# Optimization experiments

Hardware: AMD Instinct MI355X
Metric: run time of the kernel (lower is better)

The kernel has to match this reference:

```python
import jax, jax.numpy as jnp
import numpy as np

N = 50000          # num nodes
NUM_HE = 10000     # num hyperedges
E = 800000         # num graph edges
INC = 800000       # num (node, hyperedge) incidences
IN_C, HID, OUT_C = 128, 128, 64
SLOPE = 0.01       # torch leaky_relu default negative slope


def _leaky(x):
    return jnp.where(x >= 0, x, SLOPE * x)


def hypergraph_conv(x, he_index, theta, bias):
    # PyG HypergraphConv (no attention, unit hyperedge weights):
    # out = D^{-1} H B^{-1} H^T (X Theta) + bias
    node_idx, he_idx = he_index[0], he_index[1]
    x = x @ theta                                            # [N, F]
    ones = jnp.ones(node_idx.shape[0], x.dtype)
    D = jax.ops.segment_sum(ones, node_idx, num_segments=N)           # node degree
    B = jax.ops.segment_sum(ones, he_idx, num_segments=NUM_HE)        # hyperedge degree
    Dinv = jnp.where(D > 0, 1.0 / D, 0.0)
    Binv = jnp.where(B > 0, 1.0 / B, 0.0)
    # node -> hyperedge
    m = jax.ops.segment_sum(x[node_idx], he_idx, num_segments=NUM_HE) * Binv[:, None]
    # hyperedge -> node
    out = jax.ops.segment_sum(m[he_idx], node_idx, num_segments=N) * Dinv[:, None]
    return out + bias


def graph_conv(x, edge_index, w_rel, b_rel, w_root):
    # PyG GraphConv (aggr='add'): out_i = W_rel * sum_{j->i} x_j + b_rel + W_root * x_i
    src, dst = edge_index[0], edge_index[1]
    agg = jax.ops.segment_sum(x[src], dst, num_segments=N)
    return agg @ w_rel + b_rel + x @ w_root


def _forward(X, edge_index, hyperedge_index,
             hc1_w, hc1_b, lin1_w, lin1_b,
             hc2_w, hc2_b, lin2_w, lin2_b,
             c1_wrel, c1_brel, c1_wroot, glin1_w, glin1_b,
             c2_wrel, c2_brel, c2_wroot, glin2_w, glin2_b,
             fc_w, fc_b):
    # dropout is identity in eval mode (and first two calls in the source discard their output)
    X = _leaky(hypergraph_conv(X, hyperedge_index, hc1_w, hc1_b) + (X @ lin1_w + lin1_b))
    X = _leaky(hypergraph_conv(X, hyperedge_index, hc2_w, hc2_b) + (X @ lin2_w + lin2_b))
    X = _leaky(graph_conv(X, edge_index, c1_wrel, c1_brel, c1_wroot) + (X @ glin1_w + glin1_b))
    X = _leaky(graph_conv(X, edge_index, c2_wrel, c2_brel, c2_wroot) + (X @ glin2_w + glin2_b))
    y = X @ fc_w + fc_b
    return X, y


def setup_inputs() -> dict:
    key = jax.random.key(0)
    ks = jax.random.split(key, 32)
    s = 0.02
    inp = {
        'X': jax.random.normal(ks[0], (N, IN_C), jnp.float32),
        'edge_index': jnp.stack([
            jax.random.randint(ks[1], (E,), 0, N),
            jax.random.randint(ks[2], (E,), 0, N)]).astype(jnp.int64),
        'hyperedge_index': jnp.stack([
            jax.random.randint(ks[3], (INC,), 0, N),
            jax.random.randint(ks[4], (INC,), 0, NUM_HE)]).astype(jnp.int64),
        'hc1_w': jax.random.normal(ks[5], (IN_C, HID), jnp.float32) * s,
        'hc1_b': jnp.zeros((HID,), jnp.float32),
        'lin1_w': jax.random.normal(ks[6], (IN_C, HID), jnp.float32) * s,
        'lin1_b': jnp.zeros((HID,), jnp.float32),
        'hc2_w': jax.random.normal(ks[7], (HID, HID), jnp.float32) * s,
        'hc2_b': jnp.zeros((HID,), jnp.float32),
        'lin2_w': jax.random.normal(ks[8], (HID, HID), jnp.float32) * s,
        'lin2_b': jnp.zeros((HID,), jnp.float32),
        'c1_wrel': jax.random.normal(ks[9], (HID, HID), jnp.float32) * s,
        'c1_brel': jnp.zeros((HID,), jnp.float32),
        'c1_wroot': jax.random.normal(ks[10], (HID, HID), jnp.float32) * s,
        'glin1_w': jax.random.normal(ks[11], (HID, HID), jnp.float32) * s,
        'glin1_b': jnp.zeros((HID,), jnp.float32),
        'c2_wrel': jax.random.normal(ks[12], (HID, HID), jnp.float32) * s,
        'c2_brel': jnp.zeros((HID,), jnp.float32),
        'c2_wroot': jax.random.normal(ks[13], (HID, HID), jnp.float32) * s,
        'glin2_w': jax.random.normal(ks[14], (HID, HID), jnp.float32) * s,
        'glin2_b': jnp.zeros((HID,), jnp.float32),
        'fc_w': jax.random.normal(ks[15], (HID, OUT_C), jnp.float32) * s,
        'fc_b': jnp.zeros((OUT_C,), jnp.float32),
    }
    return inp


def reference(X, edge_index, hyperedge_index,
              hc1_w, hc1_b, lin1_w, lin1_b,
              hc2_w, hc2_b, lin2_w, lin2_b,
              c1_wrel, c1_brel, c1_wroot, glin1_w, glin1_b,
              c2_wrel, c2_brel, c2_wroot, glin2_w, glin2_b,
              fc_w, fc_b):
    return _forward(X, edge_index, hyperedge_index,
                    hc1_w, hc1_b, lin1_w, lin1_b,
                    hc2_w, hc2_b, lin2_w, lin2_b,
                    c1_wrel, c1_brel, c1_wroot, glin1_w, glin1_b,
                    c2_wrel, c2_brel, c2_wroot, glin2_w, glin2_b,
                    fc_w, fc_b)
```

## Files before the change

kernel.cpp:

```cpp
#include <hip/hip_runtime.h>

#define NN 50000
#define HECNT 10000
#define EE 800000
#define II 800000
#define NBK 128
#define CHUNK 4096
#define BKCAP 8192

typedef _Float16 half8 __attribute__((ext_vector_type(8)));
typedef float f32x4    __attribute__((ext_vector_type(4)));

__global__ void detect_k(const int* __restrict__ EIX, const int* __restrict__ HIX,
                         int* __restrict__ flags) {
    __shared__ int o0, o1;
    int tid = threadIdx.x;
    if (tid == 0) { o0 = 0; o1 = 0; }
    __syncthreads();
    atomicOr(&o0, EIX[2 * tid + 1]);
    atomicOr(&o1, HIX[2 * tid + 1]);
    __syncthreads();
    if (tid == 0) { flags[0] = (o0 == 0); flags[1] = (o1 == 0); }
}

__device__ __forceinline__ int ld_idx(const int* p, long long pos, int is64) {
    return is64 ? p[pos * 2] : p[(int)pos];
}

__device__ __forceinline__ void task_info(int t, int& n, int& cbase, int& obase) {
    if (t == 0)      { n = HECNT; cbase = 0;           obase = 0; }
    else if (t == 1) { n = NN;    cbase = HECNT;       obase = HECNT + 1; }
    else             { n = NN;    cbase = HECNT + NN;  obase = HECNT + NN + 2; }
}

__device__ __forceinline__ void ld_edge(int t, long long i,
                                        const int* EIX, const int* HIX,
                                        int f0, int f1, int& d, int& v) {
    int rng;
    if (t == 0)      { d = ld_idx(HIX, (long long)II + i, f1); v = ld_idx(HIX, i, f1); rng = HECNT; }
    else if (t == 1) { d = ld_idx(HIX, i, f1); v = ld_idx(HIX, (long long)II + i, f1); rng = NN; }
    else             { d = ld_idx(EIX, (long long)EE + i, f0); v = ld_idx(EIX, i, f0); rng = NN; }
    if ((unsigned)d >= (unsigned)rng || (unsigned)v >= 65536u) d = -1;
}

__global__ void binit_k(int* __restrict__ bcur) {
    int i = blockIdx.x * 256 + threadIdx.x;
    if (i < 3 * NBK) bcur[i] = i * BKCAP;
}

__global__ __launch_bounds__(256) void bin_k(const int* __restrict__ EIX,
                                             const int* __restrict__ HIX,
                                             const int* __restrict__ flags,
                                             int* __restrict__ bcur,
                                             unsigned* __restrict__ pairs) {
    int t = blockIdx.y;
    __shared__ int hcnt[NBK], hstart[NBK], hrun[NBK], gbase[NBK];
    __shared__ int stot;
    __shared__ unsigned stage[CHUNK];
    int tid = threadIdx.x;
    int n, cb, ob; task_info(t, n, cb, ob);
    int span = (n + NBK - 1) / NBK;
    long long base = (long long)blockIdx.x * CHUNK;
    int f0 = flags[0], f1 = flags[1];

    for (int i = tid; i < NBK; i += 256) { hcnt[i] = 0; hrun[i] = 0; }
    __syncthreads();

    int d[16], v[16], b[16];
    #pragma unroll
    for (int j = 0; j < 16; j++) {
        long long i = base + j * 256 + tid;
        int dd = -1, vv = 0;
        if (i < EE) ld_edge(t, i, EIX, HIX, f0, f1, dd, vv);
        d[j] = dd; v[j] = vv;
        if (dd >= 0) { b[j] = dd / span; atomicAdd(&hcnt[b[j]], 1); }
    }
    __syncthreads();

    if (tid < NBK) gbase[tid] = hcnt[tid] ? atomicAdd(&bcur[t * NBK + tid], hcnt[tid]) : 0;
    if (tid < NBK) hstart[tid] = hcnt[tid];
    __syncthreads();
    for (int o = 1; o < NBK; o <<= 1) {
        int u = 0;
        if (tid < NBK && tid >= o) u = hstart[tid - o];
        __syncthreads();
        if (tid < NBK) hstart[tid] += u;
        __syncthreads();
    }
    if (tid == NBK - 1) stot = hstart[tid];
    __syncthreads();
    if (tid < NBK) hstart[tid] -= hcnt[tid];
    __syncthreads();

    #pragma unroll
    for (int j = 0; j < 16; j++) {
        if (d[j] >= 0) {
            int p = hstart[b[j]] + atomicAdd(&hrun[b[j]], 1);
            stage[p] = ((unsigned)d[j] << 16) | (unsigned)v[j];
        }
    }
    __syncthreads();

    int total = stot;
    for (int i = tid; i < total; i += 256) {
        int lo = 0, hi = NBK - 1;
        while (lo < hi) { int mid = (lo + hi + 1) >> 1; if (hstart[mid] <= i) lo = mid; else hi = mid - 1; }
        int pos = gbase[lo] + (i - hstart[lo]);
        if (pos < (t * NBK + lo + 1) * BKCAP)
            pairs[pos] = stage[i];
    }
}

__global__ __launch_bounds__(256) void count_k(const int* __restrict__ bcur,
                                               const unsigned* __restrict__ pairs,
                                               int* __restrict__ counts) {
    int idx = blockIdx.x;
    int t = idx / NBK, b = idx % NBK;
    int n, cb, ob; task_info(t, n, cb, ob);
    int span = (n + NBK - 1) / NBK;
    int dlo = min(b * span, n), dhi = min(dlo + span, n);
    __shared__ int hist[400];
    int tid = threadIdx.x;
    for (int i = tid; i < dhi - dlo; i += 256) hist[i] = 0;
    __syncthreads();
    int cnt = min(bcur[idx] - idx * BKCAP, BKCAP);
    const unsigned* pw = pairs + (size_t)idx * BKCAP;
    for (int i = tid; i < cnt; i += 256) {
        int dl = (int)(pw[i] >> 16) - dlo;
        if ((unsigned)dl < (unsigned)(dhi - dlo)) atomicAdd(&hist[dl], 1);
    }
    __syncthreads();
    for (int i = tid; i < dhi - dlo; i += 256) counts[cb + dlo + i] = hist[i];
}

__global__ __launch_bounds__(256) void scan_p1(const int* __restrict__ counts,
                                               int* __restrict__ bsums) {
    int t = blockIdx.y;
    int n, cb, ob; task_info(t, n, cb, ob);
    int base = blockIdx.x * 1024 + threadIdx.x * 4;
    int s = 0;
    #pragma unroll
    for (int j = 0; j < 4; j++) { int i = base + j; if (i < n) s += counts[cb + i]; }
    __shared__ int red[256];
    red[threadIdx.x] = s; __syncthreads();
    for (int o = 128; o > 0; o >>= 1) {
        if (threadIdx.x < o) red[threadIdx.x] += red[threadIdx.x + o];
        __syncthreads();
    }
    if (threadIdx.x == 0) bsums[t * 64 + blockIdx.x] = red[0];
}

__global__ void scan_p2(int* __restrict__ bsums, int* __restrict__ offs) {
    int t = blockIdx.y;
    int n, cb, ob; task_info(t, n, cb, ob);
    int lane = threadIdx.x;
    int nb = (n + 1023) / 1024;
    int v = (lane < nb) ? bsums[t * 64 + lane] : 0;
    int incl = v;
    for (int d = 1; d < 64; d <<= 1) {
        int u = __shfl_up(incl, (unsigned)d, 64);
        if (lane >= d) incl += u;
    }
    bsums[t * 64 + lane] = incl - v;
    int total = __shfl(incl, 63, 64);
    if (lane == 0) offs[ob + n] = total;
}

__global__ __launch_bounds__(256) void scan_p3(const int* __restrict__ counts,
                                               const int* __restrict__ bsums,
                                               int* __restrict__ offs) {
    int t = blockIdx.y;
    int n, cb, ob; task_info(t, n, cb, ob);
    int tid = threadIdx.x;
    int base = blockIdx.x * 1024 + tid * 4;
    int c[4]; int s = 0;
    #pragma unroll
    for (int j = 0; j < 4; j++) { int i = base + j; c[j] = (i < n) ? counts[cb + i] : 0; s += c[j]; }
    __shared__ int sc[256];
    sc[tid] = s; __syncthreads();
    for (int o = 1; o < 256; o <<= 1) {
        int v = (tid >= o) ? sc[tid - o] : 0;
        __syncthreads();
        sc[tid] += v;
        __syncthreads();
    }
    int excl = sc[tid] - s;
    int p = bsums[t * 64 + blockIdx.x] + excl;
    #pragma unroll
    for (int j = 0; j < 4; j++) {
        int i = base + j;
        if (i < n) { offs[ob + i] = p; p += c[j]; }
    }
}

__global__ __launch_bounds__(256) void unbin_k(const int* __restrict__ offs,
                                               const unsigned* __restrict__ pairs,
                                               int* __restrict__ vals) {
    int idx = blockIdx.x;
    int t = idx / NBK, b = idx % NBK;
    int n, cb, ob; task_info(t, n, cb, ob);
    int span = (n + NBK - 1) / NBK;
    int dlo = min(b * span, n), dhi = min(dlo + span, n);
    if (dhi <= dlo) return;
    int p0 = offs[ob + dlo], p1 = offs[ob + dhi];
    int cnt = p1 - p0;
    __shared__ int win[BKCAP];
    __shared__ int cur[400];
    int tid = threadIdx.x;
    for (int i = tid; i < dhi - dlo; i += 256) cur[i] = offs[ob + dlo + i] - p0;
    __syncthreads();
    const unsigned* pw = pairs + (size_t)idx * BKCAP;
    int* vw = vals + (size_t)t * 800000 + p0;
    if (cnt > BKCAP) cnt = BKCAP;
    for (int i = tid; i < cnt; i += 256) {
        unsigned pv = pw[i];
        int dl = (int)(pv >> 16) - dlo;
        if ((unsigned)dl < (unsigned)(dhi - dlo)) {
            int p = atomicAdd(&cur[dl], 1);
            if ((unsigned)p < (unsigned)BKCAP) win[p] = (int)(pv & 0xffffu);
        }
    }
    __syncthreads();
    for (int i = tid; i < cnt; i += 256) vw[i] = win[i];
}

__global__ __launch_bounds__(256) void gather_k(const int* __restrict__ offs,
                                                const int* __restrict__ vals,
                                                const _Float16* __restrict__ src,
                                                _Float16* __restrict__ out,
                                                int ndst, int nsrc, int scale_flag,
                                                const float* __restrict__ bias,
                                                const _Float16* __restrict__ addend,
                                                int act) {
    int wave = threadIdx.x >> 6, lane = threadIdx.x & 63;
    int sub = lane >> 4, l16 = lane & 15;
    int d = blockIdx.x * 4 + wave;
    if (d >= ndst) return;
    int beg = offs[d], end = offs[d + 1];
    int f = l16 * 8;
    float a[8] = {0.f, 0.f, 0.f, 0.f, 0.f, 0.f, 0.f, 0.f};
    auto acc_row = [&](int s) {
        if ((unsigned)s < (unsigned)nsrc) {
            half8 u = *(const half8*)(src + (size_t)s * 128 + f);
            #pragma unroll
            for (int j = 0; j < 8; j++) a[j] += (float)u[j];
        }
    };
    int e = beg + sub;
    for (; e + 4 < end; e += 8) {
        int s0 = vals[e], s1 = vals[e + 4];
        acc_row(s0); acc_row(s1);
    }
    if (e < end) acc_row(vals[e]);
    #pragma unroll
    for (int j = 0; j < 8; j++) {
        a[j] += __shfl_xor(a[j], 16, 64);
        a[j] += __shfl_xor(a[j], 32, 64);
    }
    if (sub == 0) {
        if (scale_flag) {
            int c = end - beg;
            float iv = (c > 0) ? 1.f / (float)c : 0.f;
            #pragma unroll
            for (int j = 0; j < 8; j++) a[j] *= iv;
        }
        if (bias) {
            f32x4 b0 = *(const f32x4*)(bias + f);
            f32x4 b1 = *(const f32x4*)(bias + f + 4);
            #pragma unroll
            for (int j = 0; j < 4; j++) { a[j] += b0[j]; a[4 + j] += b1[j]; }
        }
        if (addend) {
            half8 u = *(const half8*)(addend + (size_t)d * 128 + f);
            #pragma unroll
            for (int j = 0; j < 8; j++) a[j] += (float)u[j];
        }
        if (act) {
            #pragma unroll
            for (int j = 0; j < 8; j++) a[j] = (a[j] >= 0.f) ? a[j] : 0.01f * a[j];
        }
        half8 o;
        #pragma unroll
        for (int j = 0; j < 8; j++) o[j] = (_Float16)a[j];
        *(half8*)(out + (size_t)d * 128 + f) = o;
    }
}

__global__ __launch_bounds__(256) void wprep_k(const float* __restrict__ hc1_w, const float* __restrict__ lin1_w,
                                               const float* __restrict__ hc2_w, const float* __restrict__ lin2_w,
                                               const float* __restrict__ c1_wrel, const float* __restrict__ c1_wroot,
                                               const float* __restrict__ glin1_w,
                                               const float* __restrict__ c2_wrel, const float* __restrict__ c2_wroot,
                                               const float* __restrict__ glin2_w,
                                               const float* __restrict__ fc_w,
                                               _Float16* __restrict__ F) {
    int set = blockIdx.y;
    int nfrag = (set == 4) ? 1024 : 4096;
    int NT = (set < 2) ? 16 : (set == 4 ? 4 : 8);
    int fid = blockIdx.x * 256 + threadIdx.x;
    if (fid >= nfrag) return;
    int lane = fid & 63;
    int tile = fid >> 6;
    int nt = tile % NT, ks = tile / NT;
    int n = nt * 16 + (lane & 15);
    int kbase = ks * 32 + (lane >> 4) * 8;
    _Float16* dst = F + (size_t)set * 32768 + (size_t)fid * 8;
    #pragma unroll
    for (int j = 0; j < 8; j++) {
        int k = kbase + j;
        float w;
        if (set == 0)      w = (n < 128) ? hc1_w[k * 128 + n] : lin1_w[k * 128 + n - 128];
        else if (set == 1) w = (n < 128) ? hc2_w[k * 128 + n] : lin2_w[k * 128 + n - 128];
        else if (set == 2) w = (k < 128) ? c1_wrel[k * 128 + n]
                                         : c1_wroot[(k - 128) * 128 + n] + glin1_w[(k - 128) * 128 + n];
        else if (set == 3) w = (k < 128) ? c2_wrel[k * 128 + n]
                                         : c2_wroot[(k - 128) * 128 + n] + glin2_w[(k - 128) * 128 + n];
        else               w = fc_w[k * 64 + n];
        dst[j] = (_Float16)w;
    }
}

template <typename AT>
__global__ __launch_bounds__(256) void gemm2_k(const AT* __restrict__ A,
                                               const half8* __restrict__ Bf,
                                               const float* __restrict__ b2,
                                               _Float16* __restrict__ O1,
                                               _Float16* __restrict__ O2,
                                               int M) {
    constexpr int K = 128, NT = 16;
    int tid = threadIdx.x;
    int wave = tid >> 6, lane = tid & 63;
    int quad = lane >> 4, l16 = lane & 15;
    int rowbase = blockIdx.x * 64 + wave * 16;
    int row = rowbase + l16;

    f32x4 acc[NT];
    f32x4 zero4 = {0.f, 0.f, 0.f, 0.f};
    #pragma unroll
    for (int nt = 0; nt < NT; nt++) acc[nt] = zero4;

    #pragma unroll
    for (int ks = 0; ks < 4; ks++) {
        int k0 = ks * 32 + quad * 8;
        half8 af = {0, 0, 0, 0, 0, 0, 0, 0};
        if (row < M) {
            if constexpr (sizeof(AT) == 4) {
                const float* ap = (const float*)A + (size_t)row * K + k0;
                float4 x0 = *(const float4*)ap;
                float4 x1 = *(const float4*)(ap + 4);
                af = half8{(_Float16)x0.x, (_Float16)x0.y, (_Float16)x0.z, (_Float16)x0.w,
                           (_Float16)x1.x, (_Float16)x1.y, (_Float16)x1.z, (_Float16)x1.w};
            } else {
                af = *(const half8*)((const _Float16*)A + (size_t)row * K + k0);
            }
        }
        #pragma unroll
        for (int nt = 0; nt < NT; nt++) {
            half8 bfr = Bf[(ks * NT + nt) * 64 + lane];
            acc[nt] = __builtin_amdgcn_mfma_f32_16x16x32_f16(af, bfr, acc[nt], 0, 0, 0);
        }
    }

    #pragma unroll
    for (int nt = 0; nt < NT; nt++) {
        int col = nt * 16 + l16;
        bool second = (col >= 128);
        int c = second ? col - 128 : col;
        float bv = second ? b2[c] : 0.f;
        _Float16* O = second ? O2 : O1;
        #pragma unroll
        for (int r = 0; r < 4; r++) {
            int rr = rowbase + quad * 4 + r;
            if (rr < M) O[(size_t)rr * 128 + c] = (_Float16)(acc[nt][r] + bv);
        }
    }
}

__global__ __launch_bounds__(256) void gemmk2_k(const _Float16* __restrict__ A0,
                                                const _Float16* A1,
                                                const half8* __restrict__ Bf,
                                                const float* __restrict__ brel,
                                                const float* __restrict__ blin,
                                                float* __restrict__ Cf,
                                                _Float16* Ch,
                                                int M) {
    constexpr int NT = 8;
    int tid = threadIdx.x;
    int wave = tid >> 6, lane = tid & 63;
    int quad = lane >> 4, l16 = lane & 15;
    int rowbase = blockIdx.x * 64 + wave * 16;
    int row = rowbase + l16;

    f32x4 acc[NT];
    f32x4 zero4 = {0.f, 0.f, 0.f, 0.f};
    #pragma unroll
    for (int nt = 0; nt < NT; nt++) acc[nt] = zero4;

    #pragma unroll
    for (int ks = 0; ks < 8; ks++) {
        int k0 = ks * 32 + quad * 8;
        const _Float16* Asel = (k0 < 128) ? A0 : A1;
        int ka = k0 & 127;
        half8 af = {0, 0, 0, 0, 0, 0, 0, 0};
        if (row < M) af = *(const half8*)(Asel + (size_t)row * 128 + ka);
        #pragma unroll
        for (int nt = 0; nt < NT; nt++) {
            half8 bfr = Bf[(ks * NT + nt) * 64 + lane];
            acc[nt] = __builtin_amdgcn_mfma_f32_16x16x32_f16(af, bfr, acc[nt], 0, 0, 0);
        }
    }

    #pragma unroll
    for (int nt = 0; nt < NT; nt++) {
        int col = nt * 16 + l16;
        float bv = brel[col] + blin[col];
        #pragma unroll
        for (int r = 0; r < 4; r++) {
            int rr = rowbase + quad * 4 + r;
            if (rr < M) {
                float v = acc[nt][r] + bv;
                v = (v >= 0.f) ? v : 0.01f * v;
                if (Cf) Cf[(size_t)rr * 128 + col] = v;
                Ch[(size_t)rr * 128 + col] = (_Float16)v;
            }
        }
    }
}

__global__ __launch_bounds__(256) void gemmfc_k(const _Float16* __restrict__ A,
                                                const half8* __restrict__ Bf,
                                                const float* __restrict__ bias,
                                                float* __restrict__ C,
                                                int M) {
    constexpr int K = 128, N = 64, NT = 4;
    int tid = threadIdx.x;
    int wave = tid >> 6, lane = tid & 63;
    int quad = lane >> 4, l16 = lane & 15;
    int rowbase = blockIdx.x * 64 + wave * 16;
    int row = rowbase + l16;

    f32x4 acc[NT];
    f32x4 zero4 = {0.f, 0.f, 0.f, 0.f};
    #pragma unroll
    for (int nt = 0; nt < NT; nt++) acc[nt] = zero4;

    #pragma unroll
    for (int ks = 0; ks < 4; ks++) {
        int k0 = ks * 32 + quad * 8;
        half8 af = {0, 0, 0, 0, 0, 0, 0, 0};
        if (row < M) af = *(const half8*)(A + (size_t)row * K + k0);
        #pragma unroll
        for (int nt = 0; nt < NT; nt++) {
            half8 bfr = Bf[(ks * NT + nt) * 64 + lane];
            acc[nt] = __builtin_amdgcn_mfma_f32_16x16x32_f16(af, bfr, acc[nt], 0, 0, 0);
        }
    }

    #pragma unroll
    for (int nt = 0; nt < NT; nt++) {
        int col = nt * 16 + l16;
        float bv = bias[col];
        #pragma unroll
        for (int r = 0; r < 4; r++) {
            int rr = rowbase + quad * 4 + r;
            if (rr < M) C[(size_t)rr * N + col] = acc[nt][r] + bv;
        }
    }
}

extern "C" void kernel_launch(void* const* d_in, const int* in_sizes, int n_in,
                              void* d_out, int out_size, void* d_ws, size_t ws_size,
                              hipStream_t stream) {
    const float* X       = (const float*)d_in[0];
    const int*   EIX     = (const int*)d_in[1];
    const int*   HIX     = (const int*)d_in[2];
    const float* hc1_w   = (const float*)d_in[3];
    const float* hc1_b   = (const float*)d_in[4];
    const float* lin1_w  = (const float*)d_in[5];
    const float* lin1_b  = (const float*)d_in[6];
    const float* hc2_w   = (const float*)d_in[7];
    const float* hc2_b   = (const float*)d_in[8];
    const float* lin2_w  = (const float*)d_in[9];
    const float* lin2_b  = (const float*)d_in[10];
    const float* c1_wrel = (const float*)d_in[11];
    const float* c1_brel = (const float*)d_in[12];
    const float* c1_wroot= (const float*)d_in[13];
    const float* glin1_w = (const float*)d_in[14];
    const float* glin1_b = (const float*)d_in[15];
    const float* c2_wrel = (const float*)d_in[16];
    const float* c2_brel = (const float*)d_in[17];
    const float* c2_wroot= (const float*)d_in[18];
    const float* glin2_w = (const float*)d_in[19];
    const float* glin2_b = (const float*)d_in[20];
    const float* fc_w    = (const float*)d_in[21];
    const float* fc_b    = (const float*)d_in[22];

    char* wsp = (char*)d_ws;
    size_t off = 0;
    auto carve = [&](size_t bytes) -> char* {
        char* p = wsp + off;
        off = (off + bytes + 255) & ~(size_t)255;
        return p;
    };
    int*   flags  = (int*)carve(16);
    int*   counts = (int*)carve(110000 * 4);
    int*   offs   = (int*)carve(110003 * 4);
    int*   bsums  = (int*)carve(192 * 4);
    int*   bcur   = (int*)carve(3 * NBK * 4);
    int*   vals   = (int*)carve(2400000 * 4);
    _Float16* F   = (_Float16*)carve((4 * 32768 + 8192) * 2);
    char*  U      = carve((size_t)NN * 128 * 2 * 2);
    _Float16* P  = (_Float16*)U;
    _Float16* L  = (_Float16*)(U + (size_t)NN * 128 * 2);
    unsigned* pairs = (unsigned*)U;
    _Float16* MH = (_Float16*)carve((size_t)HECNT * 128 * 2);
    _Float16* XA = (_Float16*)carve((size_t)NN * 128 * 2);

    float* XO = (float*)d_out;
    float* YO = XO + (size_t)NN * 128;

    const half8* F0 = (const half8*)F;
    const half8* F1 = (const half8*)(F + 32768);
    const half8* F2 = (const half8*)(F + 2 * 32768);
    const half8* F3 = (const half8*)(F + 3 * 32768);
    const half8* F4 = (const half8*)(F + 4 * 32768);

    detect_k<<<1, 256, 0, stream>>>(EIX, HIX, flags);
    binit_k<<<2, 256, 0, stream>>>(bcur);
    wprep_k<<<dim3(16, 5), 256, 0, stream>>>(hc1_w, lin1_w, hc2_w, lin2_w,
                                             c1_wrel, c1_wroot, glin1_w,
                                             c2_wrel, c2_wroot, glin2_w, fc_w, F);
    bin_k<<<dim3((EE + CHUNK - 1) / CHUNK, 3), 256, 0, stream>>>(EIX, HIX, flags, bcur, pairs);
    count_k<<<3 * NBK, 256, 0, stream>>>(bcur, pairs, counts);
    scan_p1<<<dim3(49, 3), 256, 0, stream>>>(counts, bsums);
    scan_p2<<<dim3(1, 3), 64, 0, stream>>>(bsums, offs);
    scan_p3<<<dim3(49, 3), 256, 0, stream>>>(counts, bsums, offs);
    unbin_k<<<3 * NBK, 256, 0, stream>>>(offs, pairs, vals);

    const int* offs_he   = offs;
    const int* offs_node = offs + HECNT + 1;
    const int* offs_dst  = offs + HECNT + NN + 2;
    const int* vals_he   = vals;
    const int* vals_node = vals + 800000;
    const int* vals_dst  = vals + 1600000;

    int g64 = (NN + 63) / 64;
    int ghe = (HECNT + 3) / 4;
    int gnn = (NN + 3) / 4;

    gemm2_k<float><<<g64, 256, 0, stream>>>(X, F0, lin1_b, P, L, NN);
    gather_k<<<ghe, 256, 0, stream>>>(offs_he, vals_he, P, MH, HECNT, NN, 1, nullptr, nullptr, 0);
    gather_k<<<gnn, 256, 0, stream>>>(offs_node, vals_node, MH, XA, NN, HECNT, 1, hc1_b, L, 1);

    gemm2_k<_Float16><<<g64, 256, 0, stream>>>(XA, F1, lin2_b, P, L, NN);
    gather_k<<<ghe, 256, 0, stream>>>(offs_he, vals_he, P, MH, HECNT, NN, 1, nullptr, nullptr, 0);
    gather_k<<<gnn, 256, 0, stream>>>(offs_node, vals_node, MH, XA, NN, HECNT, 1, hc2_b, L, 1);

    gather_k<<<gnn, 256, 0, stream>>>(offs_dst, vals_dst, XA, P, NN, NN, 0, nullptr, nullptr, 0);
    gemmk2_k<<<g64, 256, 0, stream>>>(P, XA, F2, c1_brel, glin1_b, nullptr, XA, NN);

    gather_k<<<gnn, 256, 0, stream>>>(offs_dst, vals_dst, XA, P, NN, NN, 0, nullptr, nullptr, 0);
    gemmk2_k<<<g64, 256, 0, stream>>>(P, XA, F3, c2_brel, glin2_b, XO, XA, NN);

    gemmfc_k<<<g64, 256, 0, stream>>>(XA, F4, fc_b, YO, NN);
}
```

Before: 481.4 us.

## Narrow CSR indices to u16, share hyperedge loads across binning, deepen gather unroll

```diff
diff --git a/kernel.cpp b/kernel.cpp
--- a/kernel.cpp
+++ b/kernel.cpp
@@ -10,18 +10,7 @@
 
 typedef _Float16 half8 __attribute__((ext_vector_type(8)));
 typedef float f32x4    __attribute__((ext_vector_type(4)));
-
-__global__ void detect_k(const int* __restrict__ EIX, const int* __restrict__ HIX,
-                         int* __restrict__ flags) {
-    __shared__ int o0, o1;
-    int tid = threadIdx.x;
-    if (tid == 0) { o0 = 0; o1 = 0; }
-    __syncthreads();
-    atomicOr(&o0, EIX[2 * tid + 1]);
-    atomicOr(&o1, HIX[2 * tid + 1]);
-    __syncthreads();
-    if (tid == 0) { flags[0] = (o0 == 0); flags[1] = (o1 == 0); }
-}
+typedef unsigned short u16;
 
 __device__ __forceinline__ int ld_idx(const int* p, long long pos, int is64) {
     return is64 ? p[pos * 2] : p[(int)pos];
@@ -33,51 +22,130 @@
     else             { n = NN;    cbase = HECNT + NN;  obase = HECNT + NN + 2; }
 }
 
-__device__ __forceinline__ void ld_edge(int t, long long i,
-                                        const int* EIX, const int* HIX,
-                                        int f0, int f1, int& d, int& v) {
-    int rng;
-    if (t == 0)      { d = ld_idx(HIX, (long long)II + i, f1); v = ld_idx(HIX, i, f1); rng = HECNT; }
-    else if (t == 1) { d = ld_idx(HIX, i, f1); v = ld_idx(HIX, (long long)II + i, f1); rng = NN; }
-    else             { d = ld_idx(EIX, (long long)EE + i, f0); v = ld_idx(EIX, i, f0); rng = NN; }
-    if ((unsigned)d >= (unsigned)rng || (unsigned)v >= 65536u) d = -1;
-}
-
-__global__ void binit_k(int* __restrict__ bcur) {
-    int i = blockIdx.x * 256 + threadIdx.x;
+__global__ void detect_binit_k(const int* __restrict__ EIX, const int* __restrict__ HIX,
+                               int* __restrict__ flags, int* __restrict__ bcur) {
+    int tid = threadIdx.x;
+    int i = blockIdx.x * 256 + tid;
     if (i < 3 * NBK) bcur[i] = i * BKCAP;
-}
-
-__global__ __launch_bounds__(256) void bin_k(const int* __restrict__ EIX,
-                                             const int* __restrict__ HIX,
-                                             const int* __restrict__ flags,
-                                             int* __restrict__ bcur,
-                                             unsigned* __restrict__ pairs) {
-    int t = blockIdx.y;
+    if (blockIdx.x == 0) {
+        __shared__ int o0, o1;
+        if (tid == 0) { o0 = 0; o1 = 0; }
+        __syncthreads();
+        atomicOr(&o0, EIX[2 * tid + 1]);
+        atomicOr(&o1, HIX[2 * tid + 1]);
+        __syncthreads();
+        if (tid == 0) { flags[0] = (o0 == 0); flags[1] = (o1 == 0); }
+    }
+}
+
+__global__ __launch_bounds__(256) void bin01_k(const int* __restrict__ HIX,
+                                               const int* __restrict__ flags,
+                                               int* __restrict__ bcur,
+                                               unsigned* __restrict__ pairs) {
+    __shared__ int hcnt[2][NBK], hstart[2][NBK], hrun[2][NBK], gbase[2][NBK];
+    __shared__ int stot[2];
+    __shared__ unsigned stage[2][CHUNK];
+    int tid = threadIdx.x;
+    long long base = (long long)blockIdx.x * CHUNK;
+    int f1 = flags[1];
+    const int span0 = (HECNT + NBK - 1) / NBK;
+    const int span1 = (NN + NBK - 1) / NBK;
+
+    for (int i = tid; i < NBK; i += 256) {
+        hcnt[0][i] = 0; hcnt[1][i] = 0; hrun[0][i] = 0; hrun[1][i] = 0;
+    }
+    __syncthreads();
+
+    int nd[16], he[16];
+    #pragma unroll
+    for (int j = 0; j < 16; j++) {
+        long long i = base + j * 256 + tid;
+        int n_ = -1, h_ = -1;
+        if (i < II) {
+            n_ = ld_idx(HIX, i, f1);
+            h_ = ld_idx(HIX, (long long)II + i, f1);
+            if ((unsigned)n_ >= (unsigned)NN || (unsigned)h_ >= (unsigned)HECNT) { n_ = -1; h_ = -1; }
+        }
+        nd[j] = n_; he[j] = h_;
+        if (h_ >= 0) { atomicAdd(&hcnt[0][h_ / span0], 1); atomicAdd(&hcnt[1][n_ / span1], 1); }
+    }
+    __syncthreads();
+
+    if (tid < NBK) {
+        gbase[0][tid] = hcnt[0][tid] ? atomicAdd(&bcur[tid], hcnt[0][tid]) : 0;
+        gbase[1][tid] = hcnt[1][tid] ? atomicAdd(&bcur[NBK + tid], hcnt[1][tid]) : 0;
+        hstart[0][tid] = hcnt[0][tid];
+        hstart[1][tid] = hcnt[1][tid];
+    }
+    __syncthreads();
+    for (int o = 1; o < NBK; o <<= 1) {
+        int u0 = 0, u1 = 0;
+        if (tid < NBK && tid >= o) { u0 = hstart[0][tid - o]; u1 = hstart[1][tid - o]; }
+        __syncthreads();
+        if (tid < NBK) { hstart[0][tid] += u0; hstart[1][tid] += u1; }
+        __syncthreads();
+    }
+    if (tid == NBK - 1) { stot[0] = hstart[0][tid]; stot[1] = hstart[1][tid]; }
+    __syncthreads();
+    if (tid < NBK) { hstart[0][tid] -= hcnt[0][tid]; hstart[1][tid] -= hcnt[1][tid]; }
+    __syncthreads();
+
+    #pragma unroll
+    for (int j = 0; j < 16; j++) {
+        if (he[j] >= 0) {
+            int b0 = he[j] / span0;
+            int p0 = hstart[0][b0] + atomicAdd(&hrun[0][b0], 1);
+            stage[0][p0] = ((unsigned)he[j] << 16) | (unsigned)nd[j];
+            int b1 = nd[j] / span1;
+            int p1 = hstart[1][b1] + atomicAdd(&hrun[1][b1], 1);
+            stage[1][p1] = ((unsigned)nd[j] << 16) | (unsigned)he[j];
+        }
+    }
+    __syncthreads();
+
+    for (int tt = 0; tt < 2; tt++) {
+        int total = stot[tt];
+        for (int i = tid; i < total; i += 256) {
+            int lo = 0, hi = NBK - 1;
+            while (lo < hi) { int mid = (lo + hi + 1) >> 1; if (hstart[tt][mid] <= i) lo = mid; else hi = mid - 1; }
+            int pos = gbase[tt][lo] + (i - hstart[tt][lo]);
+            if (pos < (tt * NBK + lo + 1) * BKCAP)
+                pairs[pos] = stage[tt][i];
+        }
+    }
+}
+
+__global__ __launch_bounds__(256) void bin2_k(const int* __restrict__ EIX,
+                                              const int* __restrict__ flags,
+                                              int* __restrict__ bcur,
+                                              unsigned* __restrict__ pairs) {
     __shared__ int hcnt[NBK], hstart[NBK], hrun[NBK], gbase[NBK];
     __shared__ int stot;
     __shared__ unsigned stage[CHUNK];
     int tid = threadIdx.x;
-    int n, cb, ob; task_info(t, n, cb, ob);
-    int span = (n + NBK - 1) / NBK;
     long long base = (long long)blockIdx.x * CHUNK;
-    int f0 = flags[0], f1 = flags[1];
+    int f0 = flags[0];
+    const int span = (NN + NBK - 1) / NBK;
 
     for (int i = tid; i < NBK; i += 256) { hcnt[i] = 0; hrun[i] = 0; }
     __syncthreads();
 
-    int d[16], v[16], b[16];
+    int d[16], v[16];
     #pragma unroll
     for (int j = 0; j < 16; j++) {
         long long i = base + j * 256 + tid;
-        int dd = -1, vv = 0;
-        if (i < EE) ld_edge(t, i, EIX, HIX, f0, f1, dd, vv);
+        int dd = -1, vv = -1;
+        if (i < EE) {
+            dd = ld_idx(EIX, (long long)EE + i, f0);
+            vv = ld_idx(EIX, i, f0);
+            if ((unsigned)dd >= (unsigned)NN || (unsigned)vv >= (unsigned)NN) dd = -1;
+        }
         d[j] = dd; v[j] = vv;
-        if (dd >= 0) { b[j] = dd / span; atomicAdd(&hcnt[b[j]], 1); }
-    }
-    __syncthreads();
-
-    if (tid < NBK) gbase[tid] = hcnt[tid] ? atomicAdd(&bcur[t * NBK + tid], hcnt[tid]) : 0;
+        if (dd >= 0) atomicAdd(&hcnt[dd / span], 1);
+    }
+    __syncthreads();
+
+    if (tid < NBK) gbase[tid] = hcnt[tid] ? atomicAdd(&bcur[2 * NBK + tid], hcnt[tid]) : 0;
     if (tid < NBK) hstart[tid] = hcnt[tid];
     __syncthreads();
     for (int o = 1; o < NBK; o <<= 1) {
@@ -95,7 +163,8 @@
     #pragma unroll
     for (int j = 0; j < 16; j++) {
         if (d[j] >= 0) {
-            int p = hstart[b[j]] + atomicAdd(&hrun[b[j]], 1);
+            int b = d[j] / span;
+            int p = hstart[b] + atomicAdd(&hrun[b], 1);
             stage[p] = ((unsigned)d[j] << 16) | (unsigned)v[j];
         }
     }
@@ -106,7 +175,7 @@
         int lo = 0, hi = NBK - 1;
         while (lo < hi) { int mid = (lo + hi + 1) >> 1; if (hstart[mid] <= i) lo = mid; else hi = mid - 1; }
         int pos = gbase[lo] + (i - hstart[lo]);
-        if (pos < (t * NBK + lo + 1) * BKCAP)
+        if (pos < (2 * NBK + lo + 1) * BKCAP)
             pairs[pos] = stage[i];
     }
 }
@@ -195,7 +264,7 @@
 
 __global__ __launch_bounds__(256) void unbin_k(const int* __restrict__ offs,
                                                const unsigned* __restrict__ pairs,
-                                               int* __restrict__ vals) {
+                                               u16* __restrict__ vals) {
     int idx = blockIdx.x;
     int t = idx / NBK, b = idx % NBK;
     int n, cb, ob; task_info(t, n, cb, ob);
@@ -204,20 +273,20 @@
     if (dhi <= dlo) return;
     int p0 = offs[ob + dlo], p1 = offs[ob + dhi];
     int cnt = p1 - p0;
-    __shared__ int win[BKCAP];
+    __shared__ u16 win[BKCAP];
     __shared__ int cur[400];
     int tid = threadIdx.x;
     for (int i = tid; i < dhi - dlo; i += 256) cur[i] = offs[ob + dlo + i] - p0;
     __syncthreads();
     const unsigned* pw = pairs + (size_t)idx * BKCAP;
-    int* vw = vals + (size_t)t * 800000 + p0;
+    u16* vw = vals + (size_t)t * 800000 + p0;
     if (cnt > BKCAP) cnt = BKCAP;
     for (int i = tid; i < cnt; i += 256) {
         unsigned pv = pw[i];
         int dl = (int)(pv >> 16) - dlo;
         if ((unsigned)dl < (unsigned)(dhi - dlo)) {
             int p = atomicAdd(&cur[dl], 1);
-            if ((unsigned)p < (unsigned)BKCAP) win[p] = (int)(pv & 0xffffu);
+            if ((unsigned)p < (unsigned)BKCAP) win[p] = (u16)(pv & 0xffffu);
         }
     }
     __syncthreads();
@@ -225,7 +294,7 @@
 }
 
 __global__ __launch_bounds__(256) void gather_k(const int* __restrict__ offs,
-                                                const int* __restrict__ vals,
+                                                const u16* __restrict__ vals,
                                                 const _Float16* __restrict__ src,
                                                 _Float16* __restrict__ out,
                                                 int ndst, int nsrc, int scale_flag,
@@ -247,11 +316,11 @@
         }
     };
     int e = beg + sub;
-    for (; e + 4 < end; e += 8) {
-        int s0 = vals[e], s1 = vals[e + 4];
-        acc_row(s0); acc_row(s1);
-    }
-    if (e < end) acc_row(vals[e]);
+    for (; e + 12 < end; e += 16) {
+        int s0 = vals[e], s1 = vals[e + 4], s2 = vals[e + 8], s3 = vals[e + 12];
+        acc_row(s0); acc_row(s1); acc_row(s2); acc_row(s3);
+    }
+    for (; e < end; e += 4) acc_row(vals[e]);
     #pragma unroll
     for (int j = 0; j < 8; j++) {
         a[j] += __shfl_xor(a[j], 16, 64);
@@ -507,7 +576,7 @@
     int*   offs   = (int*)carve(110003 * 4);
     int*   bsums  = (int*)carve(192 * 4);
     int*   bcur   = (int*)carve(3 * NBK * 4);
-    int*   vals   = (int*)carve(2400000 * 4);
+    u16*   vals   = (u16*)carve(2400000 * 2);
     _Float16* F   = (_Float16*)carve((4 * 32768 + 8192) * 2);
     char*  U      = carve((size_t)NN * 128 * 2 * 2);
     _Float16* P  = (_Float16*)U;
@@ -525,12 +594,12 @@
     const half8* F3 = (const half8*)(F + 3 * 32768);
     const half8* F4 = (const half8*)(F + 4 * 32768);
 
-    detect_k<<<1, 256, 0, stream>>>(EIX, HIX, flags);
-    binit_k<<<2, 256, 0, stream>>>(bcur);
+    detect_binit_k<<<2, 256, 0, stream>>>(EIX, HIX, flags, bcur);
     wprep_k<<<dim3(16, 5), 256, 0, stream>>>(hc1_w, lin1_w, hc2_w, lin2_w,
                                              c1_wrel, c1_wroot, glin1_w,
                                              c2_wrel, c2_wroot, glin2_w, fc_w, F);
-    bin_k<<<dim3((EE + CHUNK - 1) / CHUNK, 3), 256, 0, stream>>>(EIX, HIX, flags, bcur, pairs);
+    bin01_k<<<(II + CHUNK - 1) / CHUNK, 256, 0, stream>>>(HIX, flags, bcur, pairs);
+    bin2_k<<<(EE + CHUNK - 1) / CHUNK, 256, 0, stream>>>(EIX, flags, bcur, pairs);
     count_k<<<3 * NBK, 256, 0, stream>>>(bcur, pairs, counts);
     scan_p1<<<dim3(49, 3), 256, 0, stream>>>(counts, bsums);
     scan_p2<<<dim3(1, 3), 64, 0, stream>>>(bsums, offs);
@@ -540,9 +609,9 @@
     const int* offs_he   = offs;
     const int* offs_node = offs + HECNT + 1;
     const int* offs_dst  = offs + HECNT + NN + 2;
-    const int* vals_he   = vals;
-    const int* vals_node = vals + 800000;
-    const int* vals_dst  = vals + 1600000;
+    const u16* vals_he   = vals;
+    const u16* vals_node = vals + 800000;
+    const u16* vals_dst  = vals + 1600000;
 
     int g64 = (NN + 63) / 64;
     int ghe = (HECNT + 3) / 4;
```

After: 508.1 us. 1.06x slower.

## Streamline CSR build: per-bucket scan, fused count/unbin, u16 indices, wider gather unroll

Applied to the files above, without the earlier changes.

```diff
diff --git a/kernel.cpp b/kernel.cpp
--- a/kernel.cpp
+++ b/kernel.cpp
@@ -10,18 +10,7 @@
 
 typedef _Float16 half8 __attribute__((ext_vector_type(8)));
 typedef float f32x4    __attribute__((ext_vector_type(4)));
-
-__global__ void detect_k(const int* __restrict__ EIX, const int* __restrict__ HIX,
-                         int* __restrict__ flags) {
-    __shared__ int o0, o1;
-    int tid = threadIdx.x;
-    if (tid == 0) { o0 = 0; o1 = 0; }
-    __syncthreads();
-    atomicOr(&o0, EIX[2 * tid + 1]);
-    atomicOr(&o1, HIX[2 * tid + 1]);
-    __syncthreads();
-    if (tid == 0) { flags[0] = (o0 == 0); flags[1] = (o1 == 0); }
-}
+typedef unsigned short u16;
 
 __device__ __forceinline__ int ld_idx(const int* p, long long pos, int is64) {
     return is64 ? p[pos * 2] : p[(int)pos];
@@ -43,9 +32,20 @@
     if ((unsigned)d >= (unsigned)rng || (unsigned)v >= 65536u) d = -1;
 }
 
-__global__ void binit_k(int* __restrict__ bcur) {
-    int i = blockIdx.x * 256 + threadIdx.x;
+__global__ void detect_binit_k(const int* __restrict__ EIX, const int* __restrict__ HIX,
+                               int* __restrict__ flags, int* __restrict__ bcur) {
+    int tid = threadIdx.x;
+    int i = blockIdx.x * 256 + tid;
     if (i < 3 * NBK) bcur[i] = i * BKCAP;
+    if (blockIdx.x == 0) {
+        __shared__ int o0, o1;
+        if (tid == 0) { o0 = 0; o1 = 0; }
+        __syncthreads();
+        atomicOr(&o0, EIX[2 * tid + 1]);
+        atomicOr(&o1, HIX[2 * tid + 1]);
+        __syncthreads();
+        if (tid == 0) { flags[0] = (o0 == 0); flags[1] = (o1 == 0); }
+    }
 }
 
 __global__ __launch_bounds__(256) void bin_k(const int* __restrict__ EIX,
@@ -66,14 +66,14 @@
     for (int i = tid; i < NBK; i += 256) { hcnt[i] = 0; hrun[i] = 0; }
     __syncthreads();
 
-    int d[16], v[16], b[16];
+    int d[16], v[16];
     #pragma unroll
     for (int j = 0; j < 16; j++) {
         long long i = base + j * 256 + tid;
         int dd = -1, vv = 0;
         if (i < EE) ld_edge(t, i, EIX, HIX, f0, f1, dd, vv);
         d[j] = dd; v[j] = vv;
-        if (dd >= 0) { b[j] = dd / span; atomicAdd(&hcnt[b[j]], 1); }
+        if (dd >= 0) atomicAdd(&hcnt[dd / span], 1);
     }
     __syncthreads();
 
@@ -95,7 +95,8 @@
     #pragma unroll
     for (int j = 0; j < 16; j++) {
         if (d[j] >= 0) {
-            int p = hstart[b[j]] + atomicAdd(&hrun[b[j]], 1);
+            int b = d[j] / span;
+            int p = hstart[b] + atomicAdd(&hrun[b], 1);
             stage[p] = ((unsigned)d[j] << 16) | (unsigned)v[j];
         }
     }
@@ -107,125 +108,101 @@
         while (lo < hi) { int mid = (lo + hi + 1) >> 1; if (hstart[mid] <= i) lo = mid; else hi = mid - 1; }
         int pos = gbase[lo] + (i - hstart[lo]);
         if (pos < (t * NBK + lo + 1) * BKCAP)
-            pairs[pos] = stage[i];
-    }
-}
-
-__global__ __launch_bounds__(256) void count_k(const int* __restrict__ bcur,
-                                               const unsigned* __restrict__ pairs,
-                                               int* __restrict__ counts) {
-    int idx = blockIdx.x;
-    int t = idx / NBK, b = idx % NBK;
-    int n, cb, ob; task_info(t, n, cb, ob);
-    int span = (n + NBK - 1) / NBK;
-    int dlo = min(b * span, n), dhi = min(dlo + span, n);
-    __shared__ int hist[400];
-    int tid = threadIdx.x;
-    for (int i = tid; i < dhi - dlo; i += 256) hist[i] = 0;
-    __syncthreads();
-    int cnt = min(bcur[idx] - idx * BKCAP, BKCAP);
-    const unsigned* pw = pairs + (size_t)idx * BKCAP;
-    for (int i = tid; i < cnt; i += 256) {
-        int dl = (int)(pw[i] >> 16) - dlo;
-        if ((unsigned)dl < (unsigned)(dhi - dlo)) atomicAdd(&hist[dl], 1);
-    }
-    __syncthreads();
-    for (int i = tid; i < dhi - dlo; i += 256) counts[cb + dlo + i] = hist[i];
-}
-
-__global__ __launch_bounds__(256) void scan_p1(const int* __restrict__ counts,
-                                               int* __restrict__ bsums) {
-    int t = blockIdx.y;
-    int n, cb, ob; task_info(t, n, cb, ob);
-    int base = blockIdx.x * 1024 + threadIdx.x * 4;
-    int s = 0;
-    #pragma unroll
-    for (int j = 0; j < 4; j++) { int i = base + j; if (i < n) s += counts[cb + i]; }
-    __shared__ int red[256];
-    red[threadIdx.x] = s; __syncthreads();
-    for (int o = 128; o > 0; o >>= 1) {
-        if (threadIdx.x < o) red[threadIdx.x] += red[threadIdx.x + o];
-        __syncthreads();
-    }
-    if (threadIdx.x == 0) bsums[t * 64 + blockIdx.x] = red[0];
-}
-
-__global__ void scan_p2(int* __restrict__ bsums, int* __restrict__ offs) {
-    int t = blockIdx.y;
-    int n, cb, ob; task_info(t, n, cb, ob);
-    int lane = threadIdx.x;
-    int nb = (n + 1023) / 1024;
-    int v = (lane < nb) ? bsums[t * 64 + lane] : 0;
-    int incl = v;
-    for (int d = 1; d < 64; d <<= 1) {
-        int u = __shfl_up(incl, (unsigned)d, 64);
-        if (lane >= d) incl += u;
-    }
-    bsums[t * 64 + lane] = incl - v;
-    int total = __shfl(incl, 63, 64);
-    if (lane == 0) offs[ob + n] = total;
-}
-
-__global__ __launch_bounds__(256) void scan_p3(const int* __restrict__ counts,
-                                               const int* __restrict__ bsums,
+            pairs[pos] = stage[lo == 0 ? i : i];
+    }
+}
+
+__global__ __launch_bounds__(384) void bscan_k(const int* __restrict__ bcur,
+                                               int* __restrict__ bbase,
                                                int* __restrict__ offs) {
-    int t = blockIdx.y;
-    int n, cb, ob; task_info(t, n, cb, ob);
-    int tid = threadIdx.x;
-    int base = blockIdx.x * 1024 + tid * 4;
-    int c[4]; int s = 0;
-    #pragma unroll
-    for (int j = 0; j < 4; j++) { int i = base + j; c[j] = (i < n) ? counts[cb + i] : 0; s += c[j]; }
-    __shared__ int sc[256];
-    sc[tid] = s; __syncthreads();
-    for (int o = 1; o < 256; o <<= 1) {
-        int v = (tid >= o) ? sc[tid - o] : 0;
-        __syncthreads();
-        sc[tid] += v;
-        __syncthreads();
-    }
-    int excl = sc[tid] - s;
-    int p = bsums[t * 64 + blockIdx.x] + excl;
-    #pragma unroll
-    for (int j = 0; j < 4; j++) {
-        int i = base + j;
-        if (i < n) { offs[ob + i] = p; p += c[j]; }
-    }
-}
-
-__global__ __launch_bounds__(256) void unbin_k(const int* __restrict__ offs,
-                                               const unsigned* __restrict__ pairs,
-                                               int* __restrict__ vals) {
+    __shared__ int sc[3 * NBK];
+    int tid = threadIdx.x;
+    int c = 0;
+    if (tid < 3 * NBK) {
+        c = bcur[tid] - tid * BKCAP;
+        c = max(0, min(c, BKCAP));
+        sc[tid] = c;
+    }
+    __syncthreads();
+    int b = tid & (NBK - 1);
+    for (int o = 1; o < NBK; o <<= 1) {
+        int u = 0;
+        if (tid < 3 * NBK && b >= o) u = sc[tid - o];
+        __syncthreads();
+        if (tid < 3 * NBK) sc[tid] += u;
+        __syncthreads();
+    }
+    if (tid < 3 * NBK) {
+        bbase[tid] = sc[tid] - c;
+        if (b == NBK - 1) {
+            int t = tid >> 7;
+            int n, cb, ob; task_info(t, n, cb, ob);
+            offs[ob + n] = sc[tid];
+        }
+    }
+}
+
+__global__ __launch_bounds__(256) void bfin_k(const int* __restrict__ bcur,
+                                              const int* __restrict__ bbase,
+                                              const unsigned* __restrict__ pairs,
+                                              int* __restrict__ offs,
+                                              u16* __restrict__ vals) {
     int idx = blockIdx.x;
     int t = idx / NBK, b = idx % NBK;
     int n, cb, ob; task_info(t, n, cb, ob);
     int span = (n + NBK - 1) / NBK;
     int dlo = min(b * span, n), dhi = min(dlo + span, n);
     if (dhi <= dlo) return;
-    int p0 = offs[ob + dlo], p1 = offs[ob + dhi];
-    int cnt = p1 - p0;
-    __shared__ int win[BKCAP];
-    __shared__ int cur[400];
-    int tid = threadIdx.x;
-    for (int i = tid; i < dhi - dlo; i += 256) cur[i] = offs[ob + dlo + i] - p0;
-    __syncthreads();
+    int nd = dhi - dlo;
+    int cnt = bcur[idx] - idx * BKCAP;
+    cnt = max(0, min(cnt, BKCAP));
+    int base = bbase[idx];
+
+    __shared__ int hist[512], sc[512], cur[400];
+    __shared__ u16 win[BKCAP];
+    int tid = threadIdx.x;
+    for (int i = tid; i < 512; i += 256) { hist[i] = 0; }
+    __syncthreads();
+
     const unsigned* pw = pairs + (size_t)idx * BKCAP;
-    int* vw = vals + (size_t)t * 800000 + p0;
-    if (cnt > BKCAP) cnt = BKCAP;
+    for (int i = tid; i < cnt; i += 256) {
+        int dl = (int)(pw[i] >> 16) - dlo;
+        if ((unsigned)dl < (unsigned)nd) atomicAdd(&hist[dl], 1);
+    }
+    __syncthreads();
+
+    int s0 = tid, s1 = tid + 256;
+    sc[s0] = hist[s0]; sc[s1] = hist[s1];
+    __syncthreads();
+    for (int o = 1; o < 512; o <<= 1) {
+        int u0 = (s0 >= o) ? sc[s0 - o] : 0;
+        int u1 = (s1 >= o) ? sc[s1 - o] : 0;
+        __syncthreads();
+        sc[s0] += u0; sc[s1] += u1;
+        __syncthreads();
+    }
+    for (int i = tid; i < nd; i += 256) {
+        int ex = sc[i] - hist[i];
+        offs[ob + dlo + i] = base + ex;
+        cur[i] = ex;
+    }
+    __syncthreads();
+
     for (int i = tid; i < cnt; i += 256) {
         unsigned pv = pw[i];
         int dl = (int)(pv >> 16) - dlo;
-        if ((unsigned)dl < (unsigned)(dhi - dlo)) {
+        if ((unsigned)dl < (unsigned)nd) {
             int p = atomicAdd(&cur[dl], 1);
-            if ((unsigned)p < (unsigned)BKCAP) win[p] = (int)(pv & 0xffffu);
-        }
-    }
-    __syncthreads();
+            if ((unsigned)p < (unsigned)BKCAP) win[p] = (u16)(pv & 0xffffu);
+        }
+    }
+    __syncthreads();
+    u16* vw = vals + (size_t)t * 800000 + base;
     for (int i = tid; i < cnt; i += 256) vw[i] = win[i];
 }
 
 __global__ __launch_bounds__(256) void gather_k(const int* __restrict__ offs,
-                                                const int* __restrict__ vals,
+                                                const u16* __restrict__ vals,
                                                 const _Float16* __restrict__ src,
                                                 _Float16* __restrict__ out,
                                                 int ndst, int nsrc, int scale_flag,
@@ -247,11 +224,11 @@
         }
     };
     int e = beg + sub;
-    for (; e + 4 < end; e += 8) {
-        int s0 = vals[e], s1 = vals[e + 4];
-        acc_row(s0); acc_row(s1);
-    }
-    if (e < end) acc_row(vals[e]);
+    for (; e + 12 < end; e += 16) {
+        int s0 = vals[e], s1 = vals[e + 4], s2 = vals[e + 8], s3 = vals[e + 12];
+        acc_row(s0); acc_row(s1); acc_row(s2); acc_row(s3);
+    }
+    for (; e < end; e += 4) acc_row(vals[e]);
     #pragma unroll
     for (int j = 0; j < 8; j++) {
         a[j] += __shfl_xor(a[j], 16, 64);
@@ -503,11 +480,10 @@
         return p;
     };
     int*   flags  = (int*)carve(16);
-    int*   counts = (int*)carve(110000 * 4);
     int*   offs   = (int*)carve(110003 * 4);
-    int*   bsums  = (int*)carve(192 * 4);
     int*   bcur   = (int*)carve(3 * NBK * 4);
-    int*   vals   = (int*)carve(2400000 * 4);
+    int*   bbase  = (int*)carve(3 * NBK * 4);
+    u16*   vals   = (u16*)carve(2400000 * 2);
     _Float16* F   = (_Float16*)carve((4 * 32768 + 8192) * 2);
     char*  U      = carve((size_t)NN * 128 * 2 * 2);
     _Float16* P  = (_Float16*)U;
@@ -525,24 +501,20 @@
     const half8* F3 = (const half8*)(F + 3 * 32768);
     const half8* F4 = (const half8*)(F + 4 * 32768);
 
-    detect_k<<<1, 256, 0, stream>>>(EIX, HIX, flags);
-    binit_k<<<2, 256, 0, stream>>>(bcur);
+    detect_binit_k<<<2, 256, 0, stream>>>(EIX, HIX, flags, bcur);
     wprep_k<<<dim3(16, 5), 256, 0, stream>>>(hc1_w, lin1_w, hc2_w, lin2_w,
                                              c1_wrel, c1_wroot, glin1_w,
                                              c2_wrel, c2_wroot, glin2_w, fc_w, F);
     bin_k<<<dim3((EE + CHUNK - 1) / CHUNK, 3), 256, 0, stream>>>(EIX, HIX, flags, bcur, pairs);
-    count_k<<<3 * NBK, 256, 0, stream>>>(bcur, pairs, counts);
-    scan_p1<<<dim3(49, 3), 256, 0, stream>>>(counts, bsums);
-    scan_p2<<<dim3(1, 3), 64, 0, stream>>>(bsums, offs);
-    scan_p3<<<dim3(49, 3), 256, 0, stream>>>(counts, bsums, offs);
-    unbin_k<<<3 * NBK, 256, 0, stream>>>(offs, pairs, vals);
+    bscan_k<<<1, 384, 0, stream>>>(bcur, bbase, offs);
+    bfin_k<<<3 * NBK, 256, 0, stream>>>(bcur, bbase, pairs, offs, vals);
 
     const int* offs_he   = offs;
     const int* offs_node = offs + HECNT + 1;
     const int* offs_dst  = offs + HECNT + NN + 2;
-    const int* vals_he   = vals;
-    const int* vals_node = vals + 800000;
-    const int* vals_dst  = vals + 1600000;
+    const u16* vals_he   = vals;
+    const u16* vals_node = vals + 800000;
+    const u16* vals_dst  = vals + 1600000;
 
     int g64 = (NN + 63) / 64;
     int ghe = (HECNT + 3) / 4;
```

After: 477.7 us. About the same (-0.8%).
